# Performance work log

Hardware: AMD Instinct MI355X
Metric: run time of the kernel (lower is better)

The kernel has to match this reference:

```python
import jax, jax.numpy as jnp
import numpy as np

B, S, D = 8, 2048, 1024
E, K = 16, 2
H = 4096
SD, SH = D // E, H // E  # 64, 256
MAX_SEQ = 2048


def setup_inputs() -> dict:
    key = jax.random.key(0)
    ks = jax.random.split(key, 5)
    x = jax.random.normal(ks[0], (B, S, D), dtype=jnp.float32)
    w_switch = jax.random.normal(ks[1], (D * MAX_SEQ, E), dtype=jnp.float32) * 0.001
    b_switch = jnp.zeros((E,), dtype=jnp.float32)
    w1 = jax.random.normal(ks[2], (E, SD, SH), dtype=jnp.float32) * (1.0 / np.sqrt(SD))
    b1 = jnp.zeros((E, SH), dtype=jnp.float32)
    w2 = jax.random.normal(ks[3], (H, D), dtype=jnp.float32) * (1.0 / np.sqrt(H))
    b2 = jnp.zeros((D,), dtype=jnp.float32)
    return {"x": x, "w_switch": w_switch, "b_switch": b_switch,
            "w1": w1, "b1": b1, "w2": w2, "b2": b2}


def reference(x, w_switch, b_switch, w1, b1, w2, b2):
    # Router: softmax over experts from flattened first MAX_SEQ tokens
    x0 = x[:, :MAX_SEQ].reshape(B, -1)                      # [B, D*MAX_SEQ]
    route_prob = jax.nn.softmax(x0 @ w_switch + b_switch)   # [B, E]
    # Top-k expert membership mask per batch element
    _, topk_idx = jax.lax.top_k(route_prob, K)              # [B, K]
    mask = jax.nn.one_hot(topk_idx, E, dtype=x.dtype).sum(axis=1)  # [B, E]
    # Per-expert linear on the expert's channel slice, masked combine
    xe = x.reshape(B, S, E, SD)                              # [B, S, E, SD]
    h = jnp.einsum('bsed,edh->bseh', xe, w1) + b1            # [B, S, E, SH]
    h = h * mask[:, None, :, None]                           # zero out non-routed
    out = h.reshape(B, S, H)                                 # [B, S, H]
    out = jax.nn.gelu(out, approximate=False)                # exact GELU (torch default)
    return out @ w2 + b2                                     # [B, S, D]
```

## Files before the change

### kernel.cpp

```cpp
#include <hip/hip_runtime.h>
#include <hip/hip_bf16.h>

#define B_  8
#define S_  2048
#define D_  1024
#define E_  16
#define SD_ 64
#define SH_ 256
#define H_  4096
#define R_  (D_ * S_)
#define NBLK_ 8192

typedef __attribute__((ext_vector_type(8))) short bf16x8;
typedef __attribute__((ext_vector_type(4))) float f32x4;

static __device__ __forceinline__ short f2bf(float f) {
    union { float f; unsigned u; } v; v.f = f;
    unsigned r = v.u + 0x7fffu + ((v.u >> 16) & 1u);
    return (short)(r >> 16);
}

__global__ void convert_w(const float* __restrict__ w1, const float* __restrict__ w2,
                          short* __restrict__ w1f, short* __restrict__ w2f) {
    int blk = blockIdx.x;
    if (blk < 128) {
        int t = blk * 256 + threadIdx.x;
        int lane = t & 63, ntile = (t >> 6) & 15, ks = (t >> 10) & 1, e = t >> 11;
        int k0 = ks * 32 + ((lane >> 4) << 3);
        int n  = (ntile << 4) + (lane & 15);
        const float* src = w1 + ((size_t)(e * 64 + k0) * 256 + n);
        bf16x8 o;
        #pragma unroll
        for (int j = 0; j < 8; ++j) o[j] = f2bf(src[(size_t)j * 256]);
        *(bf16x8*)(w1f + ((size_t)t << 3)) = o;
    } else {
        int t = (blk - 128) * 256 + threadIdx.x;
        int lane = t & 63, ntile = (t >> 6) & 63, kg = t >> 12;
        int k0 = (kg << 5) + ((lane >> 4) << 3);
        int n  = (ntile << 4) + (lane & 15);
        const float* src = w2 + ((size_t)k0 * 1024 + n);
        bf16x8 o;
        #pragma unroll
        for (int j = 0; j < 8; ++j) o[j] = f2bf(src[(size_t)j * 1024]);
        *(bf16x8*)(w2f + ((size_t)t << 3)) = o;
    }
}

__global__ __launch_bounds__(256, 4) void router_kernel(const float* __restrict__ x,
                                                        const float* __restrict__ wsw,
                                                        float* __restrict__ partials) {
    __shared__ float red[512];
    int tid = threadIdx.x;
    int wid = tid >> 6, lane = tid & 63;
    int q = lane & 3, rsub = lane >> 2;
    size_t wavebase = (((size_t)blockIdx.x << 2) + wid) << 6;
    const f32x4* wp = (const f32x4*)wsw + (wavebase << 2) + lane;

    f32x4 w0 = wp[0];
    f32x4 w1v = wp[64];
    f32x4 w2v = wp[128];
    f32x4 w3v = wp[192];
    float xv[4][8];
    #pragma unroll
    for (int b = 0; b < 8; ++b) {
        const float* xb = x + (size_t)b * R_ + wavebase + rsub;
        #pragma unroll
        for (int it = 0; it < 4; ++it)
            xv[it][b] = xb[it << 4];
    }

    float acc[8][4];
    #pragma unroll
    for (int b = 0; b < 8; ++b)
        #pragma unroll
        for (int j = 0; j < 4; ++j) acc[b][j] = 0.f;

    #define FMA4(W, IT)                                             \
        _Pragma("unroll")                                           \
        for (int b = 0; b < 8; ++b) {                               \
            float xs = xv[IT][b];                                   \
            acc[b][0] = fmaf(xs, (W)[0], acc[b][0]);                \
            acc[b][1] = fmaf(xs, (W)[1], acc[b][1]);                \
            acc[b][2] = fmaf(xs, (W)[2], acc[b][2]);                \
            acc[b][3] = fmaf(xs, (W)[3], acc[b][3]);                \
        }
    FMA4(w0, 0)
    FMA4(w1v, 1)
    FMA4(w2v, 2)
    FMA4(w3v, 3)
    #undef FMA4

    #pragma unroll
    for (int b = 0; b < 8; ++b)
        #pragma unroll
        for (int j = 0; j < 4; ++j) {
            float v = acc[b][j];
            v += __shfl_xor(v, 4);
            v += __shfl_xor(v, 8);
            v += __shfl_xor(v, 16);
            v += __shfl_xor(v, 32);
            acc[b][j] = v;
        }

    if (lane < 4) {
        #pragma unroll
        for (int b = 0; b < 8; ++b)
            #pragma unroll
            for (int j = 0; j < 4; ++j)
                red[(wid << 7) + b * 16 + q * 4 + j] = acc[b][j];
    }
    __syncthreads();
    if (tid < 128)
        partials[(size_t)blockIdx.x * 128 + tid] =
            red[tid] + red[128 + tid] + red[256 + tid] + red[384 + tid];
}

__global__ __launch_bounds__(256) void reduce_kernel(const float* __restrict__ partials,
                                                     float* __restrict__ part2) {
    __shared__ float sred[4][128];
    int j = blockIdx.x, tid = threadIdx.x;
    int col4 = tid & 31, rg = tid >> 5;
    const f32x4* p4 = (const f32x4*)partials;

    f32x4 acc = (f32x4){0.f, 0.f, 0.f, 0.f};
    #pragma unroll
    for (int p = 0; p < 8; ++p) {
        f32x4 v = p4[(size_t)(j * 64 + p * 8 + rg) * 32 + col4];
        acc[0] += v[0]; acc[1] += v[1]; acc[2] += v[2]; acc[3] += v[3];
    }
    #pragma unroll
    for (int k = 0; k < 4; ++k) acc[k] += __shfl_xor(acc[k], 32);

    int wid = tid >> 6, lane = tid & 63;
    if (lane < 32) {
        #pragma unroll
        for (int k = 0; k < 4; ++k) sred[wid][lane * 4 + k] = acc[k];
    }
    __syncthreads();
    if (tid < 128)
        part2[(size_t)j * 128 + tid] =
            sred[0][tid] + sred[1][tid] + sred[2][tid] + sred[3][tid];
}

__global__ __launch_bounds__(128) void topk_kernel(const float* __restrict__ part2,
                                                   const float* __restrict__ bsw,
                                                   int* __restrict__ experts) {
    __shared__ float vlog[128];
    int tid = threadIdx.x;
    float t = 0.f;
    #pragma unroll 8
    for (int j = 0; j < 128; ++j) t += part2[(size_t)j * 128 + tid];
    vlog[tid] = t + bsw[tid & 15];
    __syncthreads();
    if (tid < 8) {
        float v[16];
        #pragma unroll
        for (int e = 0; e < 16; ++e) v[e] = vlog[tid * 16 + e];
        int i0 = 0; float m0 = v[0];
        #pragma unroll
        for (int e = 1; e < 16; ++e) if (v[e] > m0) { m0 = v[e]; i0 = e; }
        int i1 = -1; float m1 = -3.4e38f;
        #pragma unroll
        for (int e = 0; e < 16; ++e) if (e != i0 && v[e] > m1) { m1 = v[e]; i1 = e; }
        experts[2 * tid]     = i0;
        experts[2 * tid + 1] = i1;
    }
}

__global__ __launch_bounds__(256, 2) void mlp_kernel(
        const float* __restrict__ x, const int* __restrict__ experts,
        const short* __restrict__ w1f, const float* __restrict__ b1,
        const short* __restrict__ w2f, const float* __restrict__ b2,
        float* __restrict__ out) {
    __shared__ short G[32][520];

    int blk  = blockIdx.x;
    int b    = blk & 7;
    int tok0 = (blk >> 3) << 5;
    int e0 = experts[2 * b], e1 = experts[2 * b + 1];
    int tid = threadIdx.x;
    int wid = tid >> 6, lane = tid & 63;
    int slot  = wid >> 1;
    int ex    = slot ? e1 : e0;
    int nhalf = wid & 1;
    int lrow = lane & 15, lk8 = (lane >> 4) << 3;

    f32x4 acc1[2][8];
    #pragma unroll
    for (int m = 0; m < 2; ++m)
        #pragma unroll
        for (int n = 0; n < 8; ++n) acc1[m][n] = (f32x4){0.f, 0.f, 0.f, 0.f};

    #pragma unroll
    for (int ks = 0; ks < 2; ++ks) {
        bf16x8 a[2];
        #pragma unroll
        for (int m = 0; m < 2; ++m) {
            const float* xp = x + (((size_t)b * S_ + tok0 + m * 16 + lrow) * D_
                                   + ex * 64 + ks * 32 + lk8);
            float4 f0 = *(const float4*)xp;
            float4 f1 = *(const float4*)(xp + 4);
            bf16x8 av;
            av[0] = f2bf(f0.x); av[1] = f2bf(f0.y); av[2] = f2bf(f0.z); av[3] = f2bf(f0.w);
            av[4] = f2bf(f1.x); av[5] = f2bf(f1.y); av[6] = f2bf(f1.z); av[7] = f2bf(f1.w);
            a[m] = av;
        }
        #pragma unroll
        for (int nt = 0; nt < 8; ++nt) {
            int ntg = nhalf * 8 + nt;
            bf16x8 bf = *(const bf16x8*)(w1f + ((((size_t)(ex * 2 + ks) * 16 + ntg) * 64 + lane) << 3));
            acc1[0][nt] = __builtin_amdgcn_mfma_f32_16x16x32_bf16(a[0], bf, acc1[0][nt], 0, 0, 0);
            acc1[1][nt] = __builtin_amdgcn_mfma_f32_16x16x32_bf16(a[1], bf, acc1[1][nt], 0, 0, 0);
        }
    }

    #pragma unroll
    for (int nt = 0; nt < 8; ++nt) {
        int ncol = (nhalf * 8 + nt) * 16 + lrow;
        float bb = b1[ex * 256 + ncol];
        #pragma unroll
        for (int m = 0; m < 2; ++m) {
            int r0 = m * 16 + ((lane >> 4) << 2);
            #pragma unroll
            for (int r = 0; r < 4; ++r) {
                float v = acc1[m][nt][r] + bb;
                v = 0.5f * v * (1.0f + erff(v * 0.70710678118f));
                G[r0 + r][slot * 256 + ncol] = f2bf(v);
            }
        }
    }
    __syncthreads();

    f32x4 acc2[2][16];
    #pragma unroll
    for (int m = 0; m < 2; ++m)
        #pragma unroll
        for (int n = 0; n < 16; ++n) acc2[m][n] = (f32x4){0.f, 0.f, 0.f, 0.f};

    for (int ks = 0; ks < 16; ++ks) {
        int e  = (ks < 8) ? e0 : e1;
        int kg = e * 8 + (ks & 7);
        bf16x8 a0 = *(const bf16x8*)&G[lrow][ks * 32 + lk8];
        bf16x8 a1 = *(const bf16x8*)&G[16 + lrow][ks * 32 + lk8];
        #pragma unroll
        for (int nt = 0; nt < 16; ++nt) {
            int ntg = wid * 16 + nt;
            bf16x8 bf = *(const bf16x8*)(w2f + ((((size_t)kg * 64 + ntg) * 64 + lane) << 3));
            acc2[0][nt] = __builtin_amdgcn_mfma_f32_16x16x32_bf16(a0, bf, acc2[0][nt], 0, 0, 0);
            acc2[1][nt] = __builtin_amdgcn_mfma_f32_16x16x32_bf16(a1, bf, acc2[1][nt], 0, 0, 0);
        }
    }

    size_t obase = ((size_t)b * S_ + tok0) * D_;
    #pragma unroll
    for (int nt = 0; nt < 16; ++nt) {
        int d = wid * 256 + nt * 16 + lrow;
        float bb = b2[d];
        #pragma unroll
        for (int m = 0; m < 2; ++m) {
            int r0 = m * 16 + ((lane >> 4) << 2);
            #pragma unroll
            for (int r = 0; r < 4; ++r)
                out[obase + (size_t)(r0 + r) * D_ + d] = acc2[m][nt][r] + bb;
        }
    }
}

extern "C" void kernel_launch(void* const* d_in, const int* in_sizes, int n_in,
                              void* d_out, int out_size, void* d_ws, size_t ws_size,
                              hipStream_t stream) {
    const float* x   = (const float*)d_in[0];
    const float* wsw = (const float*)d_in[1];
    const float* bsw = (const float*)d_in[2];
    const float* w1  = (const float*)d_in[3];
    const float* b1  = (const float*)d_in[4];
    const float* w2  = (const float*)d_in[5];
    const float* b2  = (const float*)d_in[6];
    float* out = (float*)d_out;

    int*   experts  = (int*)d_ws;
    float* partials = (float*)((char*)d_ws + 4096);
    float* part2    = (float*)((char*)d_ws + 4096 + 4194304);
    short* w1f = (short*)((char*)d_ws + 4096 + 4194304 + 65536);
    short* w2f = (short*)((char*)d_ws + 4096 + 4194304 + 65536 + 524288);

    router_kernel<<<NBLK_, 256, 0, stream>>>(x, wsw, partials);
    convert_w<<<2176, 256, 0, stream>>>(w1, w2, w1f, w2f);
    reduce_kernel<<<128, 256, 0, stream>>>(partials, part2);
    topk_kernel<<<1, 128, 0, stream>>>(part2, bsw, experts);
    mlp_kernel<<<512, 256, 0, stream>>>(x, experts, w1f, b1, w2f, b2, out);
}
```

Baseline: 131.6 us.

## Split MLP kernel work across 8 waves per block to raise occupancy

The block size of the fused MLP kernel doubles from 256 to 512 threads. Each wave now computes half as many output tiles in both GEMM stages: stage one is split by token half, and stage two by narrower output column slices. This shrinks per-wave accumulator registers so more waves can be resident to hide memory and MFMA latency. The trade-off is that each wave reuses loaded W2 fragments across fewer tiles, and the LDS A-fragment reads are duplicated across more waves.

Result: faster. 115.1 us (-12.5%).

```diff
diff --git a/kernel.cpp b/kernel.cpp
--- a/kernel.cpp
+++ b/kernel.cpp
@@ -167,7 +167,7 @@
     }
 }
 
-__global__ __launch_bounds__(256, 2) void mlp_kernel(
+__global__ __launch_bounds__(512, 4) void mlp_kernel(
         const float* __restrict__ x, const int* __restrict__ experts,
         const short* __restrict__ w1f, const float* __restrict__ b1,
         const short* __restrict__ w2f, const float* __restrict__ b2,
@@ -180,62 +180,55 @@
     int e0 = experts[2 * b], e1 = experts[2 * b + 1];
     int tid = threadIdx.x;
     int wid = tid >> 6, lane = tid & 63;
-    int slot  = wid >> 1;
-    int ex    = slot ? e1 : e0;
-    int nhalf = wid & 1;
     int lrow = lane & 15, lk8 = (lane >> 4) << 3;
-
-    f32x4 acc1[2][8];
-    #pragma unroll
-    for (int m = 0; m < 2; ++m)
-        #pragma unroll
-        for (int n = 0; n < 8; ++n) acc1[m][n] = (f32x4){0.f, 0.f, 0.f, 0.f};
-
-    #pragma unroll
-    for (int ks = 0; ks < 2; ++ks) {
-        bf16x8 a[2];
-        #pragma unroll
-        for (int m = 0; m < 2; ++m) {
-            const float* xp = x + (((size_t)b * S_ + tok0 + m * 16 + lrow) * D_
+    int r0 = (lane >> 4) << 2;
+
+    {
+        int slot  = wid >> 2;
+        int ex    = slot ? e1 : e0;
+        int nhalf = (wid >> 1) & 1;
+        int mh    = wid & 1;
+
+        f32x4 acc1[8];
+        #pragma unroll
+        for (int n = 0; n < 8; ++n) acc1[n] = (f32x4){0.f, 0.f, 0.f, 0.f};
+
+        #pragma unroll
+        for (int ks = 0; ks < 2; ++ks) {
+            const float* xp = x + (((size_t)b * S_ + tok0 + mh * 16 + lrow) * D_
                                    + ex * 64 + ks * 32 + lk8);
             float4 f0 = *(const float4*)xp;
             float4 f1 = *(const float4*)(xp + 4);
-            bf16x8 av;
-            av[0] = f2bf(f0.x); av[1] = f2bf(f0.y); av[2] = f2bf(f0.z); av[3] = f2bf(f0.w);
-            av[4] = f2bf(f1.x); av[5] = f2bf(f1.y); av[6] = f2bf(f1.z); av[7] = f2bf(f1.w);
-            a[m] = av;
-        }
+            bf16x8 a;
+            a[0] = f2bf(f0.x); a[1] = f2bf(f0.y); a[2] = f2bf(f0.z); a[3] = f2bf(f0.w);
+            a[4] = f2bf(f1.x); a[5] = f2bf(f1.y); a[6] = f2bf(f1.z); a[7] = f2bf(f1.w);
+            #pragma unroll
+            for (int nt = 0; nt < 8; ++nt) {
+                int ntg = nhalf * 8 + nt;
+                bf16x8 bf = *(const bf16x8*)(w1f + ((((size_t)(ex * 2 + ks) * 16 + ntg) * 64 + lane) << 3));
+                acc1[nt] = __builtin_amdgcn_mfma_f32_16x16x32_bf16(a, bf, acc1[nt], 0, 0, 0);
+            }
+        }
+
         #pragma unroll
         for (int nt = 0; nt < 8; ++nt) {
-            int ntg = nhalf * 8 + nt;
-            bf16x8 bf = *(const bf16x8*)(w1f + ((((size_t)(ex * 2 + ks) * 16 + ntg) * 64 + lane) << 3));
-            acc1[0][nt] = __builtin_amdgcn_mfma_f32_16x16x32_bf16(a[0], bf, acc1[0][nt], 0, 0, 0);
-            acc1[1][nt] = __builtin_amdgcn_mfma_f32_16x16x32_bf16(a[1], bf, acc1[1][nt], 0, 0, 0);
-        }
-    }
-
-    #pragma unroll
-    for (int nt = 0; nt < 8; ++nt) {
-        int ncol = (nhalf * 8 + nt) * 16 + lrow;
-        float bb = b1[ex * 256 + ncol];
-        #pragma unroll
-        for (int m = 0; m < 2; ++m) {
-            int r0 = m * 16 + ((lane >> 4) << 2);
+            int ncol = (nhalf * 8 + nt) * 16 + lrow;
+            float bb = b1[ex * 256 + ncol];
             #pragma unroll
             for (int r = 0; r < 4; ++r) {
-                float v = acc1[m][nt][r] + bb;
+                float v = acc1[nt][r] + bb;
                 v = 0.5f * v * (1.0f + erff(v * 0.70710678118f));
-                G[r0 + r][slot * 256 + ncol] = f2bf(v);
+                G[mh * 16 + r0 + r][slot * 256 + ncol] = f2bf(v);
             }
         }
     }
     __syncthreads();
 
-    f32x4 acc2[2][16];
+    f32x4 acc2[2][8];
     #pragma unroll
     for (int m = 0; m < 2; ++m)
         #pragma unroll
-        for (int n = 0; n < 16; ++n) acc2[m][n] = (f32x4){0.f, 0.f, 0.f, 0.f};
+        for (int n = 0; n < 8; ++n) acc2[m][n] = (f32x4){0.f, 0.f, 0.f, 0.f};
 
     for (int ks = 0; ks < 16; ++ks) {
         int e  = (ks < 8) ? e0 : e1;
@@ -243,8 +236,8 @@
         bf16x8 a0 = *(const bf16x8*)&G[lrow][ks * 32 + lk8];
         bf16x8 a1 = *(const bf16x8*)&G[16 + lrow][ks * 32 + lk8];
         #pragma unroll
-        for (int nt = 0; nt < 16; ++nt) {
-            int ntg = wid * 16 + nt;
+        for (int nt = 0; nt < 8; ++nt) {
+            int ntg = wid * 8 + nt;
             bf16x8 bf = *(const bf16x8*)(w2f + ((((size_t)kg * 64 + ntg) * 64 + lane) << 3));
             acc2[0][nt] = __builtin_amdgcn_mfma_f32_16x16x32_bf16(a0, bf, acc2[0][nt], 0, 0, 0);
             acc2[1][nt] = __builtin_amdgcn_mfma_f32_16x16x32_bf16(a1, bf, acc2[1][nt], 0, 0, 0);
@@ -253,15 +246,15 @@
 
     size_t obase = ((size_t)b * S_ + tok0) * D_;
     #pragma unroll
-    for (int nt = 0; nt < 16; ++nt) {
-        int d = wid * 256 + nt * 16 + lrow;
+    for (int nt = 0; nt < 8; ++nt) {
+        int d = wid * 128 + nt * 16 + lrow;
         float bb = b2[d];
         #pragma unroll
         for (int m = 0; m < 2; ++m) {
-            int r0 = m * 16 + ((lane >> 4) << 2);
+            int rr = m * 16 + r0;
             #pragma unroll
             for (int r = 0; r < 4; ++r)
-                out[obase + (size_t)(r0 + r) * D_ + d] = acc2[m][nt][r] + bb;
+                out[obase + (size_t)(rr + r) * D_ + d] = acc2[m][nt][r] + bb;
         }
     }
 }
@@ -288,5 +281,5 @@
     convert_w<<<2176, 256, 0, stream>>>(w1, w2, w1f, w2f);
     reduce_kernel<<<128, 256, 0, stream>>>(partials, part2);
     topk_kernel<<<1, 128, 0, stream>>>(part2, bsw, experts);
-    mlp_kernel<<<512, 256, 0, stream>>>(x, experts, w1f, b1, w2f, b2, out);
-}
+    mlp_kernel<<<512, 512, 0, stream>>>(x, experts, w1f, b1, w2f, b2, out);
+}
```
